# Kernel optimization log

Measured on AMD Instinct MI355X. Metric: run time of the kernel, lower is better.

The kernel has to match this reference:

```python
import jax, jax.numpy as jnp
import numpy as np

N_USERS, N_ITEMS, D, L = 100000, 30000, 64, 2
N = N_USERS + N_ITEMS
NNZ_ADJ, NNZ_SYM, NNZ_HERB = 4000000, 1600000, 480000


def spmm(rows, cols, vals, x, n):
    # sparse [n, m] @ dense [m, d] via gather + segment_sum
    return jax.ops.segment_sum(vals[:, None] * x[cols], rows, num_segments=n)


def setup_inputs():
    key = jax.random.key(0)
    ks = jax.random.split(key, 19)
    s = np.float32(1.0 / np.sqrt(D))  # xavier-like scale, keeps tanh unsaturated
    return {
        'user_embedding': jax.random.normal(ks[0], (N_USERS, D), jnp.float32) * s,
        'item_embedding': jax.random.normal(ks[1], (N_ITEMS, D), jnp.float32) * s,
        'adj_vals': jax.random.uniform(ks[2], (NNZ_ADJ,), jnp.float32),
        'sym_vals': jax.random.uniform(ks[3], (NNZ_SYM,), jnp.float32),
        'herb_vals': jax.random.uniform(ks[4], (NNZ_HERB,), jnp.float32),
        'Q_user': jax.random.normal(ks[5], (L, D, D), jnp.float32) * s,
        'Q_item': jax.random.normal(ks[6], (L, D, D), jnp.float32) * s,
        'W_gc_user': jax.random.normal(ks[7], (L, 2 * D, D), jnp.float32) * s,
        'W_gc_item': jax.random.normal(ks[8], (L, 2 * D, D), jnp.float32) * s,
        'b_gc_user': jax.random.normal(ks[9], (L, D), jnp.float32) * s,
        'b_gc_item': jax.random.normal(ks[10], (L, D), jnp.float32) * s,
        'M_user': jax.random.normal(ks[11], (D, D), jnp.float32) * s,
        'M_item': jax.random.normal(ks[12], (D, D), jnp.float32) * s,
        'adj_rows': jax.random.randint(ks[13], (NNZ_ADJ,), 0, N, jnp.int32),
        'adj_cols': jax.random.randint(ks[14], (NNZ_ADJ,), 0, N, jnp.int32),
        'sym_rows': jax.random.randint(ks[15], (NNZ_SYM,), 0, N_USERS, jnp.int32),
        'sym_cols': jax.random.randint(ks[16], (NNZ_SYM,), 0, N_USERS, jnp.int32),
        'herb_rows': jax.random.randint(ks[17], (NNZ_HERB,), 0, N_ITEMS, jnp.int32),
        'herb_cols': jax.random.randint(ks[18], (NNZ_HERB,), 0, N_ITEMS, jnp.int32),
    }


def reference(user_embedding, item_embedding, adj_vals, sym_vals, herb_vals,
              Q_user, Q_item, W_gc_user, W_gc_item, b_gc_user, b_gc_item,
              M_user, M_item, adj_rows, adj_cols, sym_rows, sym_cols,
              herb_rows, herb_cols):
    ego0 = jnp.concatenate([user_embedding, item_embedding], axis=0)  # [N, D]

    def graphsage_branch(Q, W, b):
        ego = ego0
        for k in range(L):  # loop over fixed small n_layers
            agg = spmm(adj_rows, adj_cols, adj_vals, ego, N)           # neighbor aggregate
            h = jnp.tanh(agg @ Q[k])                                    # Q transform
            ego = jnp.tanh(jnp.concatenate([ego, h], axis=1) @ W[k] + b[k])
            # mess_dropout = 0 -> identity (eval mode)
        nrm = jnp.sqrt(jnp.sum(ego * ego, axis=1, keepdims=True))
        return ego / jnp.maximum(nrm, 1e-12)                            # F.normalize(p=2, dim=1)

    u_all = graphsage_branch(Q_user, W_gc_user, b_gc_user)
    i_all = graphsage_branch(Q_item, W_gc_item, b_gc_item)
    u_g = u_all[:N_USERS]
    i_g = i_all[N_USERS:]

    user_pair = jnp.tanh(spmm(sym_rows, sym_cols, sym_vals, user_embedding, N_USERS) @ M_user)
    item_pair = jnp.tanh(spmm(herb_rows, herb_cols, herb_vals, item_embedding, N_ITEMS) @ M_item)

    # fusion == 'add'
    return jnp.concatenate([u_g + user_pair, i_g + item_pair], axis=0)  # [N, D]
```

## Files before the change

### kernel.cpp

```cpp
#include <hip/hip_runtime.h>
#include <hip/hip_fp16.h>

#define NU 100000
#define NI 30000
#define NT 130000
#define D  64
#define NNZ_ADJ  4000000
#define NNZ_SYM  1600000
#define NNZ_HERB 480000

#define CHUNK 2048
#define BROWS 512

#define NBLK_ADJ  1954
#define NBLK_SYM  782
#define NBLK_HERB 235

#define NBUCK_ADJ  254
#define NBUCK_SYM  196
#define NBUCK_HERB 59
#define CAP_ADJ  17000
#define CAP_SYM  9500
#define CAP_HERB 9500

#define OFF_QU0 0
#define OFF_QI0 4096
#define OFF_QU1 8192
#define OFF_QI1 12288
#define OFF_WU0 16384
#define OFF_WI0 24576
#define OFF_WU1 32768
#define OFF_WI1 40960
#define OFF_MU  49152
#define OFF_MI  53248
#define WT_ELEMS 57344

typedef _Float16 f16x8 __attribute__((ext_vector_type(8)));
typedef float f32x4 __attribute__((ext_vector_type(4)));

__device__ inline f32x4 mfma_16x16x32(f16x8 a, f16x8 b, f32x4 c) {
  return __builtin_amdgcn_mfma_f32_16x16x32_f16(a, b, c, 0, 0, 0);
}
__device__ inline f16x8 ld8h(const __half* p) { return *(const f16x8*)p; }

__device__ inline float pk_val(unsigned p) {
  return __half2float(__ushort_as_half((unsigned short)(p & 0x7fffu)));
}

__global__ __launch_bounds__(256) void binA_all(
    const int* __restrict__ r0, const int* __restrict__ c0,
    const float* __restrict__ v0, uint2* __restrict__ st0, int* __restrict__ bc0,
    const int* __restrict__ r1, const int* __restrict__ c1,
    const float* __restrict__ v1, uint2* __restrict__ st1, int* __restrict__ bc1,
    const int* __restrict__ r2, const int* __restrict__ c2,
    const float* __restrict__ v2, uint2* __restrict__ st2, int* __restrict__ bc2) {
  __shared__ int cnt[256], lexc[256], cur[256], gbase[256], wt[4];
  __shared__ uint2 lpk[CHUNK];
  int blk = blockIdx.x;
  const int* rows; const int* cols; const float* vals;
  uint2* staging; int* bcnt; int nnz, cap, base;
  if (blk < NBLK_ADJ) {
    rows = r0; cols = c0; vals = v0; staging = st0; bcnt = bc0;
    nnz = NNZ_ADJ; cap = CAP_ADJ; base = blk * CHUNK;
  } else if (blk < NBLK_ADJ + NBLK_SYM) {
    rows = r1; cols = c1; vals = v1; staging = st1; bcnt = bc1;
    nnz = NNZ_SYM; cap = CAP_SYM; base = (blk - NBLK_ADJ) * CHUNK;
  } else {
    rows = r2; cols = c2; vals = v2; staging = st2; bcnt = bc2;
    nnz = NNZ_HERB; cap = CAP_HERB; base = (blk - NBLK_ADJ - NBLK_SYM) * CHUNK;
  }
  int tid = threadIdx.x;
  int lim = min(CHUNK, nnz - base);
  cnt[tid] = 0;
  __syncthreads();
  for (int j = tid; j < lim; j += 256) {
    int r = rows[base + j];
    atomicAdd(&cnt[r >> 9], 1);
  }
  __syncthreads();
  int lane = tid & 63, w = tid >> 6;
  int v = cnt[tid];
  int s = v;
#pragma unroll
  for (int o = 1; o < 64; o <<= 1) {
    int t = __shfl_up(s, o, 64);
    if (lane >= o) s += t;
  }
  if (lane == 63) wt[w] = s;
  __syncthreads();
  int woff = 0;
  for (int j = 0; j < w; ++j) woff += wt[j];
  int exc = woff + s - v;
  lexc[tid] = exc;
  cur[tid] = exc;
  gbase[tid] = (v > 0) ? atomicAdd(&bcnt[tid], v) : 0;
  __syncthreads();
  for (int j = tid; j < lim; j += 256) {
    int r = rows[base + j];
    int b = r >> 9;
    unsigned short hv = __half_as_ushort(__float2half(vals[base + j])) & 0x7fffu;
    unsigned cv = ((unsigned)cols[base + j] << 15) | hv;
    int pos = atomicAdd(&cur[b], 1);
    lpk[pos] = make_uint2((unsigned)r, cv);
  }
  __syncthreads();
  for (int i = tid; i < lim; i += 256) {
    uint2 e = lpk[i];
    int b = (int)(e.x >> 9);
    int d = gbase[b] + (i - lexc[b]);
    if (d < cap) staging[(size_t)b * cap + d] = e;
  }
}

__global__ __launch_bounds__(256) void bucket_scan3(
    int* __restrict__ bc, int* __restrict__ bb,
    int* __restrict__ ptr0, int* __restrict__ ptr1, int* __restrict__ ptr2) {
  __shared__ int wt[4];
  int g = blockIdx.x;
  const int* bcnt = bc + g * 256;
  int* bbase = bb + g * 256;
  int nbuck = g == 0 ? NBUCK_ADJ : g == 1 ? NBUCK_SYM : NBUCK_HERB;
  int n = g == 0 ? NT : g == 1 ? NU : NI;
  int* ptr = g == 0 ? ptr0 : g == 1 ? ptr1 : ptr2;
  int tid = threadIdx.x, lane = tid & 63, w = tid >> 6;
  int v = (tid < nbuck) ? bcnt[tid] : 0;
  int s = v;
#pragma unroll
  for (int o = 1; o < 64; o <<= 1) {
    int t = __shfl_up(s, o, 64);
    if (lane >= o) s += t;
  }
  if (lane == 63) wt[w] = s;
  __syncthreads();
  int woff = 0;
  for (int j = 0; j < w; ++j) woff += wt[j];
  if (tid < nbuck) bbase[tid] = woff + s - v;
  if (tid == 0) ptr[n] = wt[0] + wt[1] + wt[2] + wt[3];
}

__global__ __launch_bounds__(256) void binB_all(
    const uint2* __restrict__ st0, const int* __restrict__ bc0,
    const int* __restrict__ bb0, unsigned* __restrict__ pk0, int* __restrict__ ptr0,
    const uint2* __restrict__ st1, const int* __restrict__ bc1,
    const int* __restrict__ bb1, unsigned* __restrict__ pk1, int* __restrict__ ptr1,
    const uint2* __restrict__ st2, const int* __restrict__ bc2,
    const int* __restrict__ bb2, unsigned* __restrict__ pk2, int* __restrict__ ptr2) {
  __shared__ int rof[512];
  __shared__ int wt[4];
  int blk = blockIdx.x, tid = threadIdx.x;
  const uint2* staging; const int* bcnt; const int* bbase;
  unsigned* pk; int* ptr; int n, cap, b;
  if (blk < NBUCK_ADJ) {
    staging = st0; bcnt = bc0; bbase = bb0; pk = pk0; ptr = ptr0;
    n = NT; cap = CAP_ADJ; b = blk;
  } else if (blk < NBUCK_ADJ + NBUCK_SYM) {
    staging = st1; bcnt = bc1; bbase = bb1; pk = pk1; ptr = ptr1;
    n = NU; cap = CAP_SYM; b = blk - NBUCK_ADJ;
  } else {
    staging = st2; bcnt = bc2; bbase = bb2; pk = pk2; ptr = ptr2;
    n = NI; cap = CAP_HERB; b = blk - NBUCK_ADJ - NBUCK_SYM;
  }
  int cntb = min(bcnt[b], cap);
  int gb = bbase[b];
  const uint2* st = staging + (size_t)b * cap;
  for (int i = tid; i < 512; i += 256) rof[i] = 0;
  __syncthreads();
  for (int i = tid; i < cntb; i += 256) atomicAdd(&rof[st[i].x & 511], 1);
  __syncthreads();
  int v0 = rof[2 * tid], v1 = rof[2 * tid + 1], pv = v0 + v1;
  int lane = tid & 63, w = tid >> 6, s = pv;
#pragma unroll
  for (int o = 1; o < 64; o <<= 1) {
    int t = __shfl_up(s, o, 64);
    if (lane >= o) s += t;
  }
  if (lane == 63) wt[w] = s;
  __syncthreads();
  int woff = 0;
  for (int j = 0; j < w; ++j) woff += wt[j];
  int exc = woff + s - pv;
  int r0 = b * BROWS + 2 * tid;
  if (r0 < n) ptr[r0] = gb + exc;
  if (r0 + 1 < n) ptr[r0 + 1] = gb + exc + v0;
  rof[2 * tid] = exc;
  rof[2 * tid + 1] = exc + v0;
  __syncthreads();
  for (int i = tid; i < cntb; i += 256) {
    uint2 e = st[i];
    int pos = atomicAdd(&rof[e.x & 511], 1);
    pk[gb + pos] = e.y;
  }
}

__global__ __launch_bounds__(256) void to_half(
    const float* __restrict__ U, const float* __restrict__ I,
    __half* __restrict__ EH) {
  int idx = blockIdx.x * 256 + threadIdx.x;
  const int ub = NU * D / 4;
  float4 v = idx < ub ? ((const float4*)U)[idx] : ((const float4*)I)[idx - ub];
  __half2* dst = (__half2*)EH + (size_t)idx * 2;
  dst[0] = __floats2half2_rn(v.x, v.y);
  dst[1] = __floats2half2_rn(v.z, v.w);
}

__global__ __launch_bounds__(256) void prep_weights(
    const float* __restrict__ Qu, const float* __restrict__ Qi,
    const float* __restrict__ Wu, const float* __restrict__ Wi,
    const float* __restrict__ Mu, const float* __restrict__ Mi,
    __half* __restrict__ WT) {
  int gid = blockIdx.x * 256 + threadIdx.x;
  if (gid >= WT_ELEMS) return;
  const float* src;
  int e, K, base;
  if (gid < 16384) {
    int m = gid >> 12; e = gid & 4095; K = 64; base = m * 4096;
    src = (m == 0) ? Qu : (m == 1) ? Qi : (m == 2) ? Qu + 4096 : Qi + 4096;
  } else if (gid < 49152) {
    int t = gid - 16384;
    int m = t >> 13; e = t & 8191; K = 128; base = 16384 + m * 8192;
    src = (m == 0) ? Wu : (m == 1) ? Wi : (m == 2) ? Wu + 8192 : Wi + 8192;
  } else {
    int t = gid - 49152;
    int m = t >> 12; e = t & 4095; K = 64; base = 49152 + m * 4096;
    src = (m == 0) ? Mu : Mi;
  }
  int k = e >> 6, c = e & 63;
  WT[base + c * K + k] = __float2half(src[(size_t)k * 64 + c]);
}

#define EDGE(p)                                        \
  {                                                    \
    __half2 x = Xb[(size_t)((p) >> 15) << XSHIFT];     \
    float vv = pk_val(p);                              \
    ax += vv * __half2float(__low2half(x));            \
    ay += vv * __half2float(__high2half(x));           \
  }

#define SPMM_BODY()                                    \
  float ax = 0.f, ay = 0.f;                            \
  int i = s;                                           \
  for (; i + 7 < e; i += 8) {                          \
    unsigned q0 = pk[i], q1 = pk[i + 1], q2 = pk[i + 2], q3 = pk[i + 3]; \
    unsigned q4 = pk[i + 4], q5 = pk[i + 5], q6 = pk[i + 6], q7 = pk[i + 7]; \
    EDGE(q0) EDGE(q1) EDGE(q2) EDGE(q3)                \
    EDGE(q4) EDGE(q5) EDGE(q6) EDGE(q7)                \
  }                                                    \
  for (; i + 3 < e; i += 4) {                          \
    unsigned q0 = pk[i], q1 = pk[i + 1], q2 = pk[i + 2], q3 = pk[i + 3]; \
    EDGE(q0) EDGE(q1) EDGE(q2) EDGE(q3)                \
  }                                                    \
  for (; i < e; ++i) { unsigned q = pk[i]; EDGE(q) }

__global__ __launch_bounds__(256) void spmm2_agg0(
    const int* __restrict__ ptr, const unsigned* __restrict__ pk,
    const __half* __restrict__ EH, __half* __restrict__ AGG0h) {
  int wid = (blockIdx.x * 256 + threadIdx.x) >> 5;
  int lane = threadIdx.x & 31;
  if (wid >= NT) return;
  const __half2* Xb = (const __half2*)EH + lane;
  int s = ptr[wid], e = ptr[wid + 1];
#define XSHIFT 5
  SPMM_BODY()
#undef XSHIFT
  ((__half2*)AGG0h)[(size_t)wid * 32 + lane] = __floats2half2_rn(ax, ay);
}

#define NROWS_FUSED (NT + NU + NI)
__global__ __launch_bounds__(256) void spmm2_fused(
    const int* __restrict__ ptr_adj, const unsigned* __restrict__ pk_adj,
    const int* __restrict__ ptr_sym, const unsigned* __restrict__ pk_sym,
    const int* __restrict__ ptr_herb, const unsigned* __restrict__ pk_herb,
    const __half* __restrict__ ECH, const __half* __restrict__ EH,
    __half* __restrict__ AGGh, __half* __restrict__ PAIR) {
  int wid = (blockIdx.x * 256 + threadIdx.x) >> 5;
  int lane = threadIdx.x & 31;
  if (wid >= NROWS_FUSED) return;
  const int* ptrg; const unsigned* pk; const __half2* Xb; __half2* Yp;
  int xshift, r;
  if (wid < NT) {
    r = wid; ptrg = ptr_adj; pk = pk_adj; xshift = 6;
    Xb = (const __half2*)(ECH + (r < NU ? 0 : 64)) + lane;
    Yp = (__half2*)AGGh + (size_t)r * 32 + lane;
  } else if (wid < NT + NU) {
    r = wid - NT; ptrg = ptr_sym; pk = pk_sym; xshift = 5;
    Xb = (const __half2*)EH + lane;
    Yp = (__half2*)PAIR + (size_t)r * 32 + lane;
  } else {
    r = wid - NT - NU; ptrg = ptr_herb; pk = pk_herb; xshift = 5;
    Xb = (const __half2*)(EH + (size_t)NU * D) + lane;
    Yp = (__half2*)(PAIR + (size_t)NU * D) + (size_t)r * 32 + lane;
  }
  int s = ptrg[r], e = ptrg[r + 1];
#define XSHIFT xshift
  SPMM_BODY()
#undef XSHIFT
  *Yp = __floats2half2_rn(ax, ay);
}

__global__ __launch_bounds__(256) void l0_mfma(
    const __half* __restrict__ AGG0h, const __half* __restrict__ EH,
    __half* __restrict__ ECH, const __half* __restrict__ WT,
    const float* __restrict__ bu, const float* __restrict__ bi) {
  __shared__ __half Hs[2][16][72];
  int tid = threadIdx.x;
  int wave = tid >> 6, lane = tid & 63;
  int rl = lane & 15, kg = lane >> 4;
  int rb = blockIdx.x * 16;
  int colg = wave * 16 + rl;

  const __half* Xr = AGG0h + (size_t)(rb + rl) * D + kg * 8;
  f16x8 ax0 = ld8h(Xr), ax1 = ld8h(Xr + 32);
  const __half* qu = WT + OFF_QU0 + (size_t)colg * 64 + kg * 8;
  const __half* qi = WT + OFF_QI0 + (size_t)colg * 64 + kg * 8;
  f32x4 hu = {0.f, 0.f, 0.f, 0.f}, hi = {0.f, 0.f, 0.f, 0.f};
  hu = mfma_16x16x32(ax0, ld8h(qu), hu);
  hu = mfma_16x16x32(ax1, ld8h(qu + 32), hu);
  hi = mfma_16x16x32(ax0, ld8h(qi), hi);
  hi = mfma_16x16x32(ax1, ld8h(qi + 32), hi);
#pragma unroll
  for (int r = 0; r < 4; ++r) {
    int row = kg * 4 + r;
    Hs[0][row][colg] = __float2half(tanhf(hu[r]));
    Hs[1][row][colg] = __float2half(tanhf(hi[r]));
  }
  __syncthreads();

  const __half* Er = EH + (size_t)(rb + rl) * D + kg * 8;
  f16x8 ae0 = ld8h(Er), ae1 = ld8h(Er + 32);
  f16x8 au0 = *(const f16x8*)&Hs[0][rl][kg * 8];
  f16x8 au1 = *(const f16x8*)&Hs[0][rl][32 + kg * 8];
  f16x8 ai0 = *(const f16x8*)&Hs[1][rl][kg * 8];
  f16x8 ai1 = *(const f16x8*)&Hs[1][rl][32 + kg * 8];
  const __half* wu = WT + OFF_WU0 + (size_t)colg * 128 + kg * 8;
  const __half* wi = WT + OFF_WI0 + (size_t)colg * 128 + kg * 8;
  f32x4 su = {0.f, 0.f, 0.f, 0.f}, si = {0.f, 0.f, 0.f, 0.f};
  su = mfma_16x16x32(ae0, ld8h(wu), su);
  su = mfma_16x16x32(ae1, ld8h(wu + 32), su);
  su = mfma_16x16x32(au0, ld8h(wu + 64), su);
  su = mfma_16x16x32(au1, ld8h(wu + 96), su);
  si = mfma_16x16x32(ae0, ld8h(wi), si);
  si = mfma_16x16x32(ae1, ld8h(wi + 32), si);
  si = mfma_16x16x32(ai0, ld8h(wi + 64), si);
  si = mfma_16x16x32(ai1, ld8h(wi + 96), si);
  float bbu = bu[colg], bbi = bi[colg];
#pragma unroll
  for (int r = 0; r < 4; ++r) {
    size_t row = (size_t)(rb + kg * 4 + r);
    ECH[row * 128 + colg] = __float2half(tanhf(su[r] + bbu));
    ECH[row * 128 + 64 + colg] = __float2half(tanhf(si[r] + bbi));
  }
}

__global__ __launch_bounds__(256) void l1_mfma(
    const __half* __restrict__ AGGh, const __half* __restrict__ ECH,
    const __half* __restrict__ PAIR, const __half* __restrict__ WT,
    int qoff, int woff, int moff,
    const float* __restrict__ b1, float* __restrict__ out,
    int row_start, int ec_off) {
  __shared__ __half Hs[16][72];
  __shared__ float Ss[16][68], Ps[16][68];
  int tid = threadIdx.x;
  int wave = tid >> 6, lane = tid & 63;
  int rl = lane & 15, kg = lane >> 4;
  int rb = row_start + blockIdx.x * 16;
  int colg = wave * 16 + rl;

  const __half* Xr = AGGh + (size_t)(rb + rl) * D + kg * 8;
  f16x8 ax0 = ld8h(Xr), ax1 = ld8h(Xr + 32);
  const __half* q1 = WT + qoff + (size_t)colg * 64 + kg * 8;
  f32x4 h = {0.f, 0.f, 0.f, 0.f};
  h = mfma_16x16x32(ax0, ld8h(q1), h);
  h = mfma_16x16x32(ax1, ld8h(q1 + 32), h);
#pragma unroll
  for (int r = 0; r < 4; ++r) Hs[kg * 4 + r][colg] = __float2half(tanhf(h[r]));
  __syncthreads();

  const __half* Er = ECH + (size_t)(rb + rl) * 128 + ec_off + kg * 8;
  f16x8 ae0 = ld8h(Er), ae1 = ld8h(Er + 32);
  f16x8 ah0 = *(const f16x8*)&Hs[rl][kg * 8];
  f16x8 ah1 = *(const f16x8*)&Hs[rl][32 + kg * 8];
  const __half* Pr = PAIR + (size_t)(rb + rl) * D + kg * 8;
  f16x8 ap0 = ld8h(Pr), ap1 = ld8h(Pr + 32);
  const __half* w1 = WT + woff + (size_t)colg * 128 + kg * 8;
  const __half* mm = WT + moff + (size_t)colg * 64 + kg * 8;
  f32x4 s = {0.f, 0.f, 0.f, 0.f}, sp = {0.f, 0.f, 0.f, 0.f};
  s = mfma_16x16x32(ae0, ld8h(w1), s);
  s = mfma_16x16x32(ae1, ld8h(w1 + 32), s);
  s = mfma_16x16x32(ah0, ld8h(w1 + 64), s);
  s = mfma_16x16x32(ah1, ld8h(w1 + 96), s);
  sp = mfma_16x16x32(ap0, ld8h(mm), sp);
  sp = mfma_16x16x32(ap1, ld8h(mm + 32), sp);
  float bb = b1[colg];
#pragma unroll
  for (int r = 0; r < 4; ++r) {
    Ss[kg * 4 + r][colg] = tanhf(s[r] + bb);
    Ps[kg * 4 + r][colg] = tanhf(sp[r]);
  }
  __syncthreads();

  int lr = tid >> 4, q = tid & 15;
  float4 v = *(float4*)&Ss[lr][q * 4];
  float4 p = *(float4*)&Ps[lr][q * 4];
  float ss = v.x * v.x + v.y * v.y + v.z * v.z + v.w * v.w;
  ss += __shfl_xor(ss, 1, 16);
  ss += __shfl_xor(ss, 2, 16);
  ss += __shfl_xor(ss, 4, 16);
  ss += __shfl_xor(ss, 8, 16);
  float inv = 1.0f / fmaxf(sqrtf(ss), 1e-12f);
  *(float4*)&out[(size_t)(rb + lr) * D + q * 4] =
      make_float4(v.x * inv + p.x, v.y * inv + p.y,
                  v.z * inv + p.z, v.w * inv + p.w);
}

extern "C" void kernel_launch(void* const* d_in, const int* in_sizes, int n_in,
                              void* d_out, int out_size, void* d_ws, size_t ws_size,
                              hipStream_t stream) {
  const float* user_emb = (const float*)d_in[0];
  const float* item_emb = (const float*)d_in[1];
  const float* adj_vals = (const float*)d_in[2];
  const float* sym_vals = (const float*)d_in[3];
  const float* herb_vals = (const float*)d_in[4];
  const float* Q_user = (const float*)d_in[5];
  const float* Q_item = (const float*)d_in[6];
  const float* W_user = (const float*)d_in[7];
  const float* W_item = (const float*)d_in[8];
  const float* b_user = (const float*)d_in[9];
  const float* b_item = (const float*)d_in[10];
  const float* M_user = (const float*)d_in[11];
  const float* M_item = (const float*)d_in[12];
  const int* adj_rows = (const int*)d_in[13];
  const int* adj_cols = (const int*)d_in[14];
  const int* sym_rows = (const int*)d_in[15];
  const int* sym_cols = (const int*)d_in[16];
  const int* herb_rows = (const int*)d_in[17];
  const int* herb_cols = (const int*)d_in[18];

  float* out = (float*)d_out;

  char* w = (char*)d_ws;
  size_t off = 0;
  auto alloc = [&](size_t bytes) -> void* {
    off = (off + 255) & ~(size_t)255;
    void* p = w + off;
    off += bytes;
    return p;
  };
  __half* EH    = (__half*)alloc((size_t)NT * D * 2);
  __half* AGG0h = (__half*)alloc((size_t)NT * D * 2);
  __half* ECH   = (__half*)alloc((size_t)NT * 128 * 2);
  __half* AGGh  = (__half*)alloc((size_t)NT * D * 2);
  int* ptr_adj  = (int*)alloc((size_t)(NT + 1) * 4);
  unsigned* pk_adj = (unsigned*)alloc((size_t)NNZ_ADJ * 4);
  int* ptr_sym  = (int*)alloc((size_t)(NU + 1) * 4);
  unsigned* pk_sym = (unsigned*)alloc((size_t)NNZ_SYM * 4);
  int* ptr_herb = (int*)alloc((size_t)(NI + 1) * 4);
  unsigned* pk_herb = (unsigned*)alloc((size_t)NNZ_HERB * 4);
  int* bc = (int*)alloc(768 * 4);
  int* bb = (int*)alloc(768 * 4);
  __half* WT = (__half*)alloc((size_t)WT_ELEMS * 2);

  uint2* st_adj  = (uint2*)ECH;
  uint2* st_sym  = (uint2*)AGG0h;
  uint2* st_herb = (uint2*)EH;

  prep_weights<<<(WT_ELEMS + 255) / 256, 256, 0, stream>>>(
      Q_user, Q_item, W_user, W_item, M_user, M_item, WT);

  hipMemsetAsync(bc, 0, 768 * 4, stream);
  binA_all<<<NBLK_ADJ + NBLK_SYM + NBLK_HERB, 256, 0, stream>>>(
      adj_rows, adj_cols, adj_vals, st_adj, bc,
      sym_rows, sym_cols, sym_vals, st_sym, bc + 256,
      herb_rows, herb_cols, herb_vals, st_herb, bc + 512);
  bucket_scan3<<<3, 256, 0, stream>>>(bc, bb, ptr_adj, ptr_sym, ptr_herb);
  binB_all<<<NBUCK_ADJ + NBUCK_SYM + NBUCK_HERB, 256, 0, stream>>>(
      st_adj, bc, bb, pk_adj, ptr_adj,
      st_sym, bc + 256, bb + 256, pk_sym, ptr_sym,
      st_herb, bc + 512, bb + 512, pk_herb, ptr_herb);

  to_half<<<NT * D / 4 / 256, 256, 0, stream>>>(user_emb, item_emb, EH);

  spmm2_agg0<<<NT / 8, 256, 0, stream>>>(ptr_adj, pk_adj, EH, AGG0h);
  l0_mfma<<<NT / 16, 256, 0, stream>>>(AGG0h, EH, ECH, WT, b_user, b_item);

  spmm2_fused<<<NROWS_FUSED / 8, 256, 0, stream>>>(
      ptr_adj, pk_adj, ptr_sym, pk_sym, ptr_herb, pk_herb,
      ECH, EH, AGGh, AGG0h);

  l1_mfma<<<NU / 16, 256, 0, stream>>>(
      AGGh, ECH, AGG0h, WT, OFF_QU1, OFF_WU1, OFF_MU, b_user + 64, out, 0, 0);
  l1_mfma<<<NI / 16, 256, 0, stream>>>(
      AGGh, ECH, AGG0h, WT, OFF_QI1, OFF_WI1, OFF_MI, b_item + 64, out, NU, 64);
}
```

Before: 445.1 us.

## Process SpMM rows with 16 lanes using 8-byte gathers and enlarge binning chunks

The SpMM kernels now give each row to 16 lanes, each loading 8 bytes (four halves) per edge, instead of 32 lanes loading a half2. This packs four rows into each 64-wide wave, cutting per-row index and pointer load overhead and widening each memory transaction. The binning chunk size is doubled, which halves the binA block count. The tradeoff is fewer lanes per row and more serial work per lane, plus a shorter unroll of 4 instead of 8.

```diff
diff --git a/kernel.cpp b/kernel.cpp
--- a/kernel.cpp
+++ b/kernel.cpp
@@ -9,12 +9,12 @@
 #define NNZ_SYM  1600000
 #define NNZ_HERB 480000
 
-#define CHUNK 2048
+#define CHUNK 4096
 #define BROWS 512
 
-#define NBLK_ADJ  1954
-#define NBLK_SYM  782
-#define NBLK_HERB 235
+#define NBLK_ADJ  977
+#define NBLK_SYM  391
+#define NBLK_HERB 118
 
 #define NBUCK_ADJ  254
 #define NBUCK_SYM  196
@@ -42,10 +42,6 @@
   return __builtin_amdgcn_mfma_f32_16x16x32_f16(a, b, c, 0, 0, 0);
 }
 __device__ inline f16x8 ld8h(const __half* p) { return *(const f16x8*)p; }
-
-__device__ inline float pk_val(unsigned p) {
-  return __half2float(__ushort_as_half((unsigned short)(p & 0x7fffu)));
-}
 
 __global__ __launch_bounds__(256) void binA_all(
     const int* __restrict__ r0, const int* __restrict__ c0,
@@ -228,73 +224,76 @@
   WT[base + c * K + k] = __float2half(src[(size_t)k * 64 + c]);
 }
 
-#define EDGE(p)                                        \
-  {                                                    \
-    __half2 x = Xb[(size_t)((p) >> 15) << XSHIFT];     \
-    float vv = pk_val(p);                              \
-    ax += vv * __half2float(__low2half(x));            \
-    ay += vv * __half2float(__high2half(x));           \
-  }
-
-#define SPMM_BODY()                                    \
-  float ax = 0.f, ay = 0.f;                            \
-  int i = s;                                           \
-  for (; i + 7 < e; i += 8) {                          \
-    unsigned q0 = pk[i], q1 = pk[i + 1], q2 = pk[i + 2], q3 = pk[i + 3]; \
-    unsigned q4 = pk[i + 4], q5 = pk[i + 5], q6 = pk[i + 6], q7 = pk[i + 7]; \
-    EDGE(q0) EDGE(q1) EDGE(q2) EDGE(q3)                \
-    EDGE(q4) EDGE(q5) EDGE(q6) EDGE(q7)                \
-  }                                                    \
-  for (; i + 3 < e; i += 4) {                          \
-    unsigned q0 = pk[i], q1 = pk[i + 1], q2 = pk[i + 2], q3 = pk[i + 3]; \
-    EDGE(q0) EDGE(q1) EDGE(q2) EDGE(q3)                \
-  }                                                    \
-  for (; i < e; ++i) { unsigned q = pk[i]; EDGE(q) }
-
-__global__ __launch_bounds__(256) void spmm2_agg0(
+#define EDGE16(p)                                                        \
+  {                                                                      \
+    uint2 xq_ = Xp[(size_t)((p) >> 15) << fshift];                       \
+    float vf_ = __half2float(__ushort_as_half(                           \
+        (unsigned short)((p) & 0x7fffu)));                               \
+    __half2 x0_ = *(__half2*)&xq_.x, x1_ = *(__half2*)&xq_.y;            \
+    a0 += vf_ * __half2float(__low2half(x0_));                           \
+    a1 += vf_ * __half2float(__high2half(x0_));                          \
+    a2 += vf_ * __half2float(__low2half(x1_));                           \
+    a3 += vf_ * __half2float(__high2half(x1_));                          \
+  }
+
+#define SPMM16_LOOP()                                                    \
+  float a0 = 0.f, a1 = 0.f, a2 = 0.f, a3 = 0.f;                          \
+  int i = s;                                                             \
+  for (; i + 3 < e; i += 4) {                                            \
+    unsigned e0_ = pk[i], e1_ = pk[i + 1], e2_ = pk[i + 2], e3_ = pk[i + 3]; \
+    EDGE16(e0_) EDGE16(e1_) EDGE16(e2_) EDGE16(e3_)                      \
+  }                                                                      \
+  for (; i < e; ++i) { unsigned eq_ = pk[i]; EDGE16(eq_) }
+
+__global__ __launch_bounds__(256) void spmm16_agg0(
     const int* __restrict__ ptr, const unsigned* __restrict__ pk,
     const __half* __restrict__ EH, __half* __restrict__ AGG0h) {
-  int wid = (blockIdx.x * 256 + threadIdx.x) >> 5;
-  int lane = threadIdx.x & 31;
-  if (wid >= NT) return;
-  const __half2* Xb = (const __half2*)EH + lane;
-  int s = ptr[wid], e = ptr[wid + 1];
-#define XSHIFT 5
-  SPMM_BODY()
-#undef XSHIFT
-  ((__half2*)AGG0h)[(size_t)wid * 32 + lane] = __floats2half2_rn(ax, ay);
-}
-
-#define NROWS_FUSED (NT + NU + NI)
-__global__ __launch_bounds__(256) void spmm2_fused(
+  int vid = (blockIdx.x * 256 + threadIdx.x) >> 6;
+  int lane = threadIdx.x & 63;
+  int grp = lane >> 4, l16 = lane & 15;
+  int r = vid * 4 + grp;
+  if (r >= NT) return;
+  const uint2* Xp = (const uint2*)EH + l16;
+  const int fshift = 4;
+  int s = ptr[r], e = ptr[r + 1];
+  SPMM16_LOOP()
+  __half2 o0 = __floats2half2_rn(a0, a1), o1 = __floats2half2_rn(a2, a3);
+  ((uint2*)AGG0h)[(size_t)r * 16 + l16] =
+      make_uint2(*(unsigned*)&o0, *(unsigned*)&o1);
+}
+
+__global__ __launch_bounds__(256) void spmm16_fused(
     const int* __restrict__ ptr_adj, const unsigned* __restrict__ pk_adj,
     const int* __restrict__ ptr_sym, const unsigned* __restrict__ pk_sym,
     const int* __restrict__ ptr_herb, const unsigned* __restrict__ pk_herb,
     const __half* __restrict__ ECH, const __half* __restrict__ EH,
     __half* __restrict__ AGGh, __half* __restrict__ PAIR) {
-  int wid = (blockIdx.x * 256 + threadIdx.x) >> 5;
-  int lane = threadIdx.x & 31;
-  if (wid >= NROWS_FUSED) return;
-  const int* ptrg; const unsigned* pk; const __half2* Xb; __half2* Yp;
-  int xshift, r;
-  if (wid < NT) {
-    r = wid; ptrg = ptr_adj; pk = pk_adj; xshift = 6;
-    Xb = (const __half2*)(ECH + (r < NU ? 0 : 64)) + lane;
-    Yp = (__half2*)AGGh + (size_t)r * 32 + lane;
-  } else if (wid < NT + NU) {
-    r = wid - NT; ptrg = ptr_sym; pk = pk_sym; xshift = 5;
-    Xb = (const __half2*)EH + lane;
-    Yp = (__half2*)PAIR + (size_t)r * 32 + lane;
+  int vid = (blockIdx.x * 256 + threadIdx.x) >> 6;
+  int lane = threadIdx.x & 63;
+  int grp = lane >> 4, l16 = lane & 15;
+  const int* ptrg; const unsigned* pk; const uint2* Xp; __half* Y;
+  int fshift, r;
+  if (vid < NT / 4) {
+    int rr = vid * 4;
+    ptrg = ptr_adj; pk = pk_adj; fshift = 5;
+    Xp = (const uint2*)(ECH + (rr < NU ? 0 : 64)) + l16;
+    Y = AGGh; r = rr + grp;
+  } else if (vid < (NT + NU) / 4) {
+    int rr = vid * 4 - NT;
+    ptrg = ptr_sym; pk = pk_sym; fshift = 4;
+    Xp = (const uint2*)EH + l16;
+    Y = PAIR; r = rr + grp;
   } else {
-    r = wid - NT - NU; ptrg = ptr_herb; pk = pk_herb; xshift = 5;
-    Xb = (const __half2*)(EH + (size_t)NU * D) + lane;
-    Yp = (__half2*)(PAIR + (size_t)NU * D) + (size_t)r * 32 + lane;
+    int rr = vid * 4 - NT - NU;
+    ptrg = ptr_herb; pk = pk_herb; fshift = 4;
+    Xp = (const uint2*)(EH + (size_t)NU * D) + l16;
+    Y = PAIR + (size_t)NU * D; r = rr + grp;
   }
   int s = ptrg[r], e = ptrg[r + 1];
-#define XSHIFT xshift
-  SPMM_BODY()
-#undef XSHIFT
-  *Yp = __floats2half2_rn(ax, ay);
+  SPMM16_LOOP()
+  __half2 o0 = __floats2half2_rn(a0, a1), o1 = __floats2half2_rn(a2, a3);
+  ((uint2*)Y)[(size_t)r * 16 + l16] =
+      make_uint2(*(unsigned*)&o0, *(unsigned*)&o1);
 }
 
 __global__ __launch_bounds__(256) void l0_mfma(
@@ -479,10 +478,10 @@
 
   to_half<<<NT * D / 4 / 256, 256, 0, stream>>>(user_emb, item_emb, EH);
 
-  spmm2_agg0<<<NT / 8, 256, 0, stream>>>(ptr_adj, pk_adj, EH, AGG0h);
+  spmm16_agg0<<<NT / 4 * 64 / 256, 256, 0, stream>>>(ptr_adj, pk_adj, EH, AGG0h);
   l0_mfma<<<NT / 16, 256, 0, stream>>>(AGG0h, EH, ECH, WT, b_user, b_item);
 
-  spmm2_fused<<<NROWS_FUSED / 8, 256, 0, stream>>>(
+  spmm16_fused<<<(NT + NU + NI) / 4 * 64 / 256, 256, 0, stream>>>(
       ptr_adj, pk_adj, ptr_sym, pk_sym, ptr_herb, pk_herb,
       ECH, EH, AGGh, AGG0h);
 
```

After: 428.3 us. -3.8%, faster.
